# Optimization experiments

Hardware: AMD Instinct MI355X
Metric: run time of the kernel (lower is better)

Reference implementation:

```python
import jax, jax.numpy as jnp
import numpy as np

B, H, OUT, L_LAYERS = 64, 1024, 512, 2
SEQ = 256
SOS_VALUE = -2.0  # predict_binary_output=False


def setup_inputs() -> dict:
    key = jax.random.key(0)
    ks = jax.random.split(key, 16)
    s_ih0 = 1.0 / np.sqrt(OUT)
    s_h = 1.0 / np.sqrt(H)
    return {
        "encoder_output": jax.random.normal(ks[0], (B, SEQ, OUT), jnp.float32),
        "h0": jax.random.normal(ks[1], (L_LAYERS, B, H), jnp.float32),
        "c0": jax.random.normal(ks[2], (L_LAYERS, B, H), jnp.float32),
        "W_ih0": jax.random.normal(ks[3], (4 * H, OUT), jnp.float32) * s_ih0,
        "W_hh0": jax.random.normal(ks[4], (4 * H, H), jnp.float32) * s_h,
        "b_ih0": jax.random.normal(ks[5], (4 * H,), jnp.float32) * s_h,
        "b_hh0": jax.random.normal(ks[6], (4 * H,), jnp.float32) * s_h,
        "W_ih1": jax.random.normal(ks[7], (4 * H, H), jnp.float32) * s_h,
        "W_hh1": jax.random.normal(ks[8], (4 * H, H), jnp.float32) * s_h,
        "b_ih1": jax.random.normal(ks[9], (4 * H,), jnp.float32) * s_h,
        "b_hh1": jax.random.normal(ks[10], (4 * H,), jnp.float32) * s_h,
        "W_fc": jax.random.normal(ks[11], (OUT, H), jnp.float32) * s_h,
        "b_fc": jax.random.normal(ks[12], (OUT,), jnp.float32) * s_h,
        "seq_length": SEQ,
    }


def _lstm_cell(x, h, c, Wih, Whh, bih, bhh):
    # PyTorch gate order: i, f, g, o
    gates = x @ Wih.T + h @ Whh.T + (bih + bhh)
    i, f, g, o = jnp.split(gates, 4, axis=-1)
    i = jax.nn.sigmoid(i)
    f = jax.nn.sigmoid(f)
    g = jnp.tanh(g)
    o = jax.nn.sigmoid(o)
    c_new = f * c + i * g
    h_new = o * jnp.tanh(c_new)
    return h_new, c_new


def reference(encoder_output, h0, c0, W_ih0, W_hh0, b_ih0, b_hh0,
              W_ih1, W_hh1, b_ih1, b_hh1, W_fc, b_fc, seq_length):
    batch = h0.shape[1]
    y_init = jnp.full((batch, OUT), SOS_VALUE, dtype=h0.dtype)  # SOS token
    layers = ((W_ih0, W_hh0, b_ih0, b_hh0), (W_ih1, W_hh1, b_ih1, b_hh1))

    def step(carry, _):
        h, c, y = carry  # h, c: (num_layers, B, H); y: (B, OUT)
        x = y
        hs, cs = [], []
        for l, (Wih, Whh, bih, bhh) in enumerate(layers):
            h_l, c_l = _lstm_cell(x, h[l], c[l], Wih, Whh, bih, bhh)
            hs.append(h_l)
            cs.append(c_l)
            x = h_l
        y_hat = jax.nn.relu(x @ W_fc.T + b_fc)
        return (jnp.stack(hs), jnp.stack(cs), y_hat), y_hat

    (_, _, _), ys = jax.lax.scan(step, (h0, c0, y_init), None, length=seq_length)
    return jnp.transpose(ys, (1, 0, 2))  # (B, seq_length, OUT)
```

## Files before the change

kernel.cpp:

```cpp
#include <hip/hip_runtime.h>
#include <stdint.h>


#define NBLK 256
#define NTHR 256
#define HDIM 1024
#define ODIM 512
#define BDIM 64
#define SEQL 256

typedef _Float16 v8h __attribute__((ext_vector_type(8)));
typedef float    v4f __attribute__((ext_vector_type(4)));

#define WL0_NS 48
#define WL1_NS 64
#define WFC_NS 32
#define WL0_OFF 0
#define WL1_OFF (WL0_NS*1024)
#define WFC_OFF (WL1_OFF + WL1_NS*1024)
#define SMEM_BYTES (WFC_OFF + WFC_NS*1024)

#define YB_SZ  (BDIM*ODIM*2)
#define HB_SZ  (BDIM*HDIM*2)

#define FH0_REL 0
#define FH1_REL (4*256*4)
#define FY_REL  (FH1_REL + 4*256*4)
#define EH0_REL (FY_REL + 4*256*4)
#define EH1_REL (EH0_REL + 4*8*64)
#define EY_REL  (EH1_REL + 4*8*64)
#define FLG_BYTES (EY_REL + 4*8*64)

__device__ __forceinline__ float fsig(float x)   { return 1.0f / (1.0f + __expf(-x)); }
__device__ __forceinline__ float ftanhf(float x) { return 1.0f - 2.0f / (__expf(2.0f*x) + 1.0f); }

__device__ __forceinline__ unsigned long long ald8(const void* p){
  return __hip_atomic_load((const unsigned long long*)p, __ATOMIC_RELAXED, __HIP_MEMORY_SCOPE_AGENT);
}
__device__ __forceinline__ unsigned int ald4(const void* p){
  return __hip_atomic_load((const unsigned int*)p, __ATOMIC_RELAXED, __HIP_MEMORY_SCOPE_AGENT);
}
__device__ __forceinline__ void ast4(void* p, unsigned int v){
  __hip_atomic_store((unsigned int*)p, v, __ATOMIC_RELAXED, __HIP_MEMORY_SCOPE_AGENT);
}

__device__ __forceinline__ void wrap_inv(){
  asm volatile("s_waitcnt vmcnt(0)\n\tbuffer_inv sc1" ::: "memory");
}

__device__ __forceinline__ void wait_word(const unsigned int* w, unsigned int tag){
  while (ald4(w) < tag) __builtin_amdgcn_s_sleep(1);
  asm volatile("" ::: "memory");
}

__device__ __forceinline__ void scan256_pub(const unsigned int* rowf, unsigned int* ew,
                                            unsigned int tag){
  const char* p = (const char*)(rowf + (threadIdx.x & 63)*4);
  while (true){
    unsigned long long a = ald8(p);
    unsigned long long b = ald8(p+8);
    unsigned int m0 = (unsigned int)a, m1 = (unsigned int)(a >> 32);
    unsigned int m2 = (unsigned int)b, m3 = (unsigned int)(b >> 32);
    unsigned int m = min(min(m0, m1), min(m2, m3));
    if (__all(m >= tag)) break;
    __builtin_amdgcn_s_sleep(1);
  }
  if ((threadIdx.x & 63) == 0) ast4(ew, tag);
  asm volatile("" ::: "memory");
}

__device__ __forceinline__ void publish(unsigned int* flag, unsigned int tag){
  asm volatile("s_waitcnt vmcnt(0)" ::: "memory");
  if ((threadIdx.x & 63) == 0) ast4(flag, tag);
}

template<int NC>
__device__ __forceinline__ v4f gemm_phase(const char* const cb[], const char* wl, v4f acc){
  v8h A[4][8];
  constexpr int PF = (NC < 3) ? NC : 3;
  #pragma unroll
  for (int p = 0; p < PF; p++){
    #pragma unroll
    for (int j = 0; j < 8; j++) A[p][j] = *(const v8h*)(cb[p] + (size_t)j*64);
  }
  #pragma unroll
  for (int c = 0; c < NC; c++){
    const int cur = c & 3, nx = (c + 3) & 3;
    if (c + 3 < NC){
      #pragma unroll
      for (int j = 0; j < 8; j++) A[nx][j] = *(const v8h*)(cb[c+3] + (size_t)j*64);
    }
    #pragma unroll
    for (int j = 0; j < 8; j++){
      v8h B = *(const v8h*)(wl + (size_t)(c*8 + j)*1024);
      acc = __builtin_amdgcn_mfma_f32_16x16x32_f16(A[cur][j], B, acc, 0, 0, 0);
    }
  }
  return acc;
}

__device__ __forceinline__ void gemm_dual4(const char* const cb[], const char* wlA,
                                           const char* wlB, v4f& accA, v4f& accB){
  v8h A[4][8];
  #pragma unroll
  for (int p = 0; p < 3; p++){
    #pragma unroll
    for (int j = 0; j < 8; j++) A[p][j] = *(const v8h*)(cb[p] + (size_t)j*64);
  }
  #pragma unroll
  for (int c = 0; c < 4; c++){
    const int cur = c & 3, nx = (c + 3) & 3;
    if (c + 3 < 4){
      #pragma unroll
      for (int j = 0; j < 8; j++) A[nx][j] = *(const v8h*)(cb[c+3] + (size_t)j*64);
    }
    #pragma unroll
    for (int j = 0; j < 8; j++){
      v8h BA = *(const v8h*)(wlA + (size_t)(c*8 + j)*1024);
      accA = __builtin_amdgcn_mfma_f32_16x16x32_f16(A[cur][j], BA, accA, 0, 0, 0);
      v8h BB = *(const v8h*)(wlB + (size_t)(c*8 + j)*1024);
      accB = __builtin_amdgcn_mfma_f32_16x16x32_f16(A[cur][j], BB, accB, 0, 0, 0);
    }
  }
}

__device__ __forceinline__ void lstm_epi_pack(v4f acc, float bias, float* cs,
                                              char* hbase, int l15, int gidx){
  #pragma unroll
  for (int r = 0; r < 4; r++){
    float v  = acc[r] + bias;
    float x1 = __shfl_xor(v, 1);
    float x2 = __shfl_xor(v, 2);
    float x3 = __shfl_xor(v, 3);
    float vi = (gidx==0)?v :(gidx==1)?x1:(gidx==2)?x2:x3;
    float vf = (gidx==1)?v :(gidx==0)?x1:(gidx==3)?x2:x3;
    float vg = (gidx==2)?v :(gidx==3)?x1:(gidx==0)?x2:x3;
    float vo = (gidx==3)?v :(gidx==2)?x1:(gidx==1)?x2:x3;
    float ii = fsig(vi), ff = fsig(vf), gg = ftanhf(vg), oo = fsig(vo);
    float cn = ff*cs[r] + ii*gg;
    cs[r] = cn;
    float hn = oo * ftanhf(cn);
    unsigned int uv = (unsigned int)__builtin_bit_cast(unsigned short, (_Float16)hn);
    unsigned int o4 = (unsigned int)__shfl_xor((int)uv, 4);
    unsigned int pr = uv | (o4 << 16);
    unsigned int o8 = (unsigned int)__shfl_xor((int)pr, 8);
    if (l15 == 0){
      unsigned long long full = (unsigned long long)pr | ((unsigned long long)o8 << 32);
      __hip_atomic_store((unsigned long long*)(hbase + (size_t)r*(HDIM*2)), full,
                         __ATOMIC_RELAXED, __HIP_MEMORY_SCOPE_AGENT);
    }
  }
}

__global__ void init_kernel(const float* __restrict__ h0,
                            _Float16* __restrict__ h0bi, _Float16* __restrict__ h1bi,
                            _Float16* __restrict__ ybi){
  int i = blockIdx.x*256 + threadIdx.x;
  if (i < BDIM*HDIM){
    h0bi[i] = (_Float16)h0[i];
    h1bi[i] = (_Float16)h0[BDIM*HDIM + i];
  }
  if (i < BDIM*ODIM) ybi[i] = (_Float16)(-2.0f);
}

__launch_bounds__(NTHR, 1)
__global__ void decoder_kernel(
    const float* __restrict__ Wih0, const float* __restrict__ Whh0,
    const float* __restrict__ bih0, const float* __restrict__ bhh0,
    const float* __restrict__ Wih1, const float* __restrict__ Whh1,
    const float* __restrict__ bih1, const float* __restrict__ bhh1,
    const float* __restrict__ Wfc,  const float* __restrict__ bfc,
    const float* __restrict__ c0in, float* __restrict__ out,
    char* __restrict__ yB, char* __restrict__ h0B, char* __restrict__ h1B,
    char* __restrict__ flg, int dmask)
{
  extern __shared__ char smem[];
  const int bid = blockIdx.x;
  const int tid = threadIdx.x;
  const int wv  = tid >> 6;
  const int ln  = tid & 63;
  const int l15 = ln & 15;
  const int lq  = ln >> 4;
  const int u0  = bid * 4;
  const int f   = bid & 7;
  const int lead_h0 = (bid < 8);
  const int lead_h1 = (bid >= 8  && bid < 16);
  const int lead_y  = (bid >= 16 && bid < 24);

  unsigned int* fh0r = (unsigned int*)(flg + FH0_REL) + wv*256;
  unsigned int* fh1r = (unsigned int*)(flg + FH1_REL) + wv*256;
  unsigned int* fyr  = (unsigned int*)(flg + FY_REL)  + wv*256;
  unsigned int* eh0  = (unsigned int*)(flg + EH0_REL + (wv*8 + f)*64);
  unsigned int* eh1  = (unsigned int*)(flg + EH1_REL + (wv*8 + f)*64);
  unsigned int* ey   = (unsigned int*)(flg + EY_REL  + (wv*8 + f)*64);

  for (int slot = tid; slot < WL0_NS*64; slot += NTHR){
    int s = slot >> 6, l = slot & 63;
    int r16 = l & 15, q = l >> 4;
    int grow = (r16 & 3)*HDIM + u0 + (r16 >> 2);
    int kb = s*32 + q*8;
    const float* src; int k0;
    if (kb < ODIM){ src = Wih0 + (size_t)grow*ODIM; k0 = kb; }
    else          { src = Whh0 + (size_t)grow*HDIM; k0 = kb - ODIM; }
    v8h hv;
    #pragma unroll
    for (int j = 0; j < 8; j++) hv[j] = (_Float16)src[k0 + j];
    *(v8h*)(smem + WL0_OFF + s*1024 + l*16) = hv;
  }
  for (int slot = tid; slot < WL1_NS*64; slot += NTHR){
    int s = slot >> 6, l = slot & 63;
    int r16 = l & 15, q = l >> 4;
    int grow = (r16 & 3)*HDIM + u0 + (r16 >> 2);
    int kb = s*32 + q*8;
    const float* src; int k0;
    if (kb < HDIM){ src = Wih1 + (size_t)grow*HDIM; k0 = kb; }
    else          { src = Whh1 + (size_t)grow*HDIM; k0 = kb - HDIM; }
    v8h hv;
    #pragma unroll
    for (int j = 0; j < 8; j++) hv[j] = (_Float16)src[k0 + j];
    *(v8h*)(smem + WL1_OFF + s*1024 + l*16) = hv;
  }
  for (int slot = tid; slot < WFC_NS*64; slot += NTHR){
    int s = slot >> 6, l = slot & 63;
    int r16 = l & 15, q = l >> 4;
    int k0 = s*32 + q*8;
    v8h hv;
    if (r16 < 2){
      const float* src = Wfc + (size_t)(bid*2 + r16)*HDIM;
      #pragma unroll
      for (int j = 0; j < 8; j++) hv[j] = (_Float16)src[k0 + j];
    } else {
      #pragma unroll
      for (int j = 0; j < 8; j++) hv[j] = (_Float16)0.0f;
    }
    *(v8h*)(smem + WFC_OFF + s*1024 + l*16) = hv;
  }
  __syncthreads();

  const int gidx = l15 & 3;
  const int unit = u0 + (l15 >> 2);
  const int growL = gidx*HDIM + unit;
  const float bias0 = bih0[growL] + bhh0[growL];
  const float bias1 = bih1[growL] + bhh1[growL];
  const float biasf = (l15 < 2) ? bfc[bid*2 + l15] : 0.f;

  const int rb = wv*16 + lq*4;
  float cs0[4], cs1[4];
  #pragma unroll
  for (int r = 0; r < 4; r++){
    int b = rb + r;
    cs0[r] = c0in[(size_t)(0*BDIM + b)*HDIM + unit];
    cs1[r] = c0in[(size_t)(1*BDIM + b)*HDIM + unit];
  }

  const int row = wv*16 + l15;
  const size_t aoffY = (size_t)row*ODIM*2 + (size_t)lq*16;
  const size_t aoffH = (size_t)row*HDIM*2 + (size_t)lq*16;
  const size_t hwoff = ((size_t)rb*HDIM + u0)*2;
  const char* wl0 = smem + WL0_OFF + ln*16;
  const char* wl1 = smem + WL1_OFF + ln*16;
  const char* wlf = smem + WFC_OFF + ln*16;
  const char* wl0r = wl0 + 16*1024;
  const char* wl1r = wl1 + 32*1024;

  v4f p0 = {0.f,0.f,0.f,0.f};
  {
    const char* hi = h0B + (size_t)dmask*HB_SZ + aoffH;
    const char* cb[4] = { hi, hi+512, hi+1024, hi+1536 };
    p0 = gemm_phase<4>(cb, wl0r, p0);
  }

  for (int t = 0; t < SEQL; t++){
    const int sp = (t - 1) & dmask;
    const int sc = t & dmask;

    if ((t & dmask) == 0) wrap_inv();

    if (t > 0){
      if (lead_y) scan256_pub(fyr, ey, (unsigned)t);
      else        wait_word(ey, (unsigned)t);
    }

    {
      const char* ysrc = yB + (size_t)sp*YB_SZ + aoffY;
      const char* cb[2] = { ysrc, ysrc+512 };
      v4f acc = gemm_phase<2>(cb, wl0, p0);
      lstm_epi_pack(acc, bias0, cs0, h0B + (size_t)sc*HB_SZ + hwoff, l15, gidx);
    }
    publish(&fh0r[bid], (unsigned)(t+1));

    v4f p1 = {0.f,0.f,0.f,0.f};
    {
      const char* hs = h1B + (size_t)sp*HB_SZ + aoffH;
      const char* cb[4] = { hs, hs+512, hs+1024, hs+1536 };
      p1 = gemm_phase<4>(cb, wl1r, p1);
      if (lead_h0) scan256_pub(fh0r, eh0, (unsigned)(t+1));
      else         wait_word(eh0, (unsigned)(t+1));
    }

    {
      const char* hs = h0B + (size_t)sc*HB_SZ + aoffH;
      const char* cb[4] = { hs, hs+512, hs+1024, hs+1536 };
      v4f np0 = {0.f,0.f,0.f,0.f};
      gemm_dual4(cb, wl1, wl0r, p1, np0);
      lstm_epi_pack(p1, bias1, cs1, h1B + (size_t)sc*HB_SZ + hwoff, l15, gidx);
      p0 = np0;
    }
    publish(&fh1r[bid], (unsigned)(t+1));

    if (lead_h1) scan256_pub(fh1r, eh1, (unsigned)(t+1));
    else         wait_word(eh1, (unsigned)(t+1));

    {
      const char* f1 = h1B + (size_t)sc*HB_SZ + aoffH;
      const char* cb[4] = { f1, f1+512, f1+1024, f1+1536 };
      v4f acc = {0.f,0.f,0.f,0.f};
      acc = gemm_phase<4>(cb, wlf, acc);
      char* ydst = yB + (size_t)sc*YB_SZ;
      #pragma unroll
      for (int r = 0; r < 4; r++){
        float v = fmaxf(acc[r] + biasf, 0.f);
        int b = rb + r;
        unsigned int uv = (unsigned int)__builtin_bit_cast(unsigned short, (_Float16)v);
        unsigned int o1 = (unsigned int)__shfl_xor((int)uv, 1);
        if (l15 == 0){
          unsigned int pr = uv | (o1 << 16);
          ast4(ydst + ((size_t)b*ODIM + bid*2)*2, pr);
        }
        if (l15 < 2) out[((size_t)b*SEQL + t)*ODIM + bid*2 + l15] = v;
      }
    }
    publish(&fyr[bid], (unsigned)(t+1));
  }
}

extern "C" void kernel_launch(void* const* d_in, const int* in_sizes, int n_in,
                              void* d_out, int out_size, void* d_ws, size_t ws_size,
                              hipStream_t stream){
  (void)in_sizes; (void)n_in; (void)out_size;

  int D = 16;
  while (D > 2 && (size_t)D*(YB_SZ + 2*HB_SZ) + FLG_BYTES > ws_size) D >>= 1;
  if ((size_t)D*(YB_SZ + 2*HB_SZ) + FLG_BYTES > ws_size) return;

  char* ws  = (char*)d_ws;
  char* yB  = ws;
  char* h0B = yB + (size_t)D*YB_SZ;
  char* h1B = h0B + (size_t)D*HB_SZ;
  char* flg = h1B + (size_t)D*HB_SZ;

  const float* h0   = (const float*)d_in[1];
  const float* c0   = (const float*)d_in[2];
  const float* Wih0 = (const float*)d_in[3];
  const float* Whh0 = (const float*)d_in[4];
  const float* bih0 = (const float*)d_in[5];
  const float* bhh0 = (const float*)d_in[6];
  const float* Wih1 = (const float*)d_in[7];
  const float* Whh1 = (const float*)d_in[8];
  const float* bih1 = (const float*)d_in[9];
  const float* bhh1 = (const float*)d_in[10];
  const float* Wfc  = (const float*)d_in[11];
  const float* bfc  = (const float*)d_in[12];
  float* out = (float*)d_out;

  (void)hipMemsetAsync(flg, 0, FLG_BYTES, stream);
  hipLaunchKernelGGL(init_kernel, dim3(256), dim3(256), 0, stream,
                     h0,
                     (_Float16*)(h0B + (size_t)(D-1)*HB_SZ),
                     (_Float16*)(h1B + (size_t)(D-1)*HB_SZ),
                     (_Float16*)(yB  + (size_t)(D-1)*YB_SZ));

  (void)hipFuncSetAttribute((const void*)decoder_kernel,
                            hipFuncAttributeMaxDynamicSharedMemorySize, SMEM_BYTES);
  hipLaunchKernelGGL(decoder_kernel, dim3(NBLK), dim3(NTHR), SMEM_BYTES, stream,
                     Wih0, Whh0, bih0, bhh0, Wih1, Whh1, bih1, bhh1,
                     Wfc, bfc, c0, out, yB, h0B, h1B, flg, D - 1);
}
```

Measured before the change: 4.919 ms.

## Replicate FC output across 8 block groups to replace global y barrier with local flags

The FC layer is now computed redundantly by 8 replica groups: each block computes 16 output columns instead of 2 and writes them into its own replica of the y buffer. Each layer-0 consumer then waits only on the 32 producers of its replica, not on a two-level scan and broadcast over all 256 blocks. This shortens the per-step synchronisation chain. The cost is 8x FC MFMA work, 8x y buffer memory and more workspace per slot. The fused dual GEMM for layer 1 and the next step's layer-0 recurrent term is also split, so h1 is published before the layer-0 precompute runs.

```diff
diff --git a/kernel.cpp b/kernel.cpp
--- a/kernel.cpp
+++ b/kernel.cpp
@@ -22,14 +22,14 @@
 
 #define YB_SZ  (BDIM*ODIM*2)
 #define HB_SZ  (BDIM*HDIM*2)
+#define SLOTSET (8*YB_SZ + 2*HB_SZ)
 
 #define FH0_REL 0
 #define FH1_REL (4*256*4)
-#define FY_REL  (FH1_REL + 4*256*4)
-#define EH0_REL (FY_REL + 4*256*4)
+#define FYX_REL (FH1_REL + 4*256*4)
+#define EH0_REL (FYX_REL + 8*4*32*4)
 #define EH1_REL (EH0_REL + 4*8*64)
-#define EY_REL  (EH1_REL + 4*8*64)
-#define FLG_BYTES (EY_REL + 4*8*64)
+#define FLG_BYTES (EH1_REL + 4*8*64)
 
 __device__ __forceinline__ float fsig(float x)   { return 1.0f / (1.0f + __expf(-x)); }
 __device__ __forceinline__ float ftanhf(float x) { return 1.0f - 2.0f / (__expf(2.0f*x) + 1.0f); }
@@ -69,6 +69,12 @@
   asm volatile("" ::: "memory");
 }
 
+__device__ __forceinline__ void scan_fyx(const unsigned int* rowf, unsigned int tag){
+  const unsigned int* p = rowf + (threadIdx.x & 31);
+  while (!__all(ald4(p) >= tag)) __builtin_amdgcn_s_sleep(1);
+  asm volatile("" ::: "memory");
+}
+
 __device__ __forceinline__ void publish(unsigned int* flag, unsigned int tag){
   asm volatile("s_waitcnt vmcnt(0)" ::: "memory");
   if ((threadIdx.x & 63) == 0) ast4(flag, tag);
@@ -97,31 +103,6 @@
     }
   }
   return acc;
-}
-
-__device__ __forceinline__ void gemm_dual4(const char* const cb[], const char* wlA,
-                                           const char* wlB, v4f& accA, v4f& accB){
-  v8h A[4][8];
-  #pragma unroll
-  for (int p = 0; p < 3; p++){
-    #pragma unroll
-    for (int j = 0; j < 8; j++) A[p][j] = *(const v8h*)(cb[p] + (size_t)j*64);
-  }
-  #pragma unroll
-  for (int c = 0; c < 4; c++){
-    const int cur = c & 3, nx = (c + 3) & 3;
-    if (c + 3 < 4){
-      #pragma unroll
-      for (int j = 0; j < 8; j++) A[nx][j] = *(const v8h*)(cb[c+3] + (size_t)j*64);
-    }
-    #pragma unroll
-    for (int j = 0; j < 8; j++){
-      v8h BA = *(const v8h*)(wlA + (size_t)(c*8 + j)*1024);
-      accA = __builtin_amdgcn_mfma_f32_16x16x32_f16(A[cur][j], BA, accA, 0, 0, 0);
-      v8h BB = *(const v8h*)(wlB + (size_t)(c*8 + j)*1024);
-      accB = __builtin_amdgcn_mfma_f32_16x16x32_f16(A[cur][j], BB, accB, 0, 0, 0);
-    }
-  }
 }
 
 __device__ __forceinline__ void lstm_epi_pack(v4f acc, float bias, float* cs,
@@ -160,7 +141,10 @@
     h0bi[i] = (_Float16)h0[i];
     h1bi[i] = (_Float16)h0[BDIM*HDIM + i];
   }
-  if (i < BDIM*ODIM) ybi[i] = (_Float16)(-2.0f);
+  if (i < BDIM*ODIM){
+    #pragma unroll
+    for (int x = 0; x < 8; x++) ybi[(size_t)x*(BDIM*ODIM) + i] = (_Float16)(-2.0f);
+  }
 }
 
 __launch_bounds__(NTHR, 1)
@@ -171,7 +155,7 @@
     const float* __restrict__ bih1, const float* __restrict__ bhh1,
     const float* __restrict__ Wfc,  const float* __restrict__ bfc,
     const float* __restrict__ c0in, float* __restrict__ out,
-    char* __restrict__ yB, char* __restrict__ h0B, char* __restrict__ h1B,
+    char* __restrict__ yX, char* __restrict__ h0B, char* __restrict__ h1B,
     char* __restrict__ flg, int dmask)
 {
   extern __shared__ char smem[];
@@ -183,16 +167,17 @@
   const int lq  = ln >> 4;
   const int u0  = bid * 4;
   const int f   = bid & 7;
+  const int j32 = bid >> 3;
+  const int dimb = j32 * 16;
   const int lead_h0 = (bid < 8);
-  const int lead_h1 = (bid >= 8  && bid < 16);
-  const int lead_y  = (bid >= 16 && bid < 24);
+  const int lead_h1 = (bid >= 8 && bid < 16);
+  const int outw = (f == 0);
 
   unsigned int* fh0r = (unsigned int*)(flg + FH0_REL) + wv*256;
   unsigned int* fh1r = (unsigned int*)(flg + FH1_REL) + wv*256;
-  unsigned int* fyr  = (unsigned int*)(flg + FY_REL)  + wv*256;
+  unsigned int* fyxr = (unsigned int*)(flg + FYX_REL) + (f*4 + wv)*32;
   unsigned int* eh0  = (unsigned int*)(flg + EH0_REL + (wv*8 + f)*64);
   unsigned int* eh1  = (unsigned int*)(flg + EH1_REL + (wv*8 + f)*64);
-  unsigned int* ey   = (unsigned int*)(flg + EY_REL  + (wv*8 + f)*64);
 
   for (int slot = tid; slot < WL0_NS*64; slot += NTHR){
     int s = slot >> 6, l = slot & 63;
@@ -223,16 +208,11 @@
   for (int slot = tid; slot < WFC_NS*64; slot += NTHR){
     int s = slot >> 6, l = slot & 63;
     int r16 = l & 15, q = l >> 4;
+    const float* src = Wfc + (size_t)(dimb + r16)*HDIM;
     int k0 = s*32 + q*8;
     v8h hv;
-    if (r16 < 2){
-      const float* src = Wfc + (size_t)(bid*2 + r16)*HDIM;
-      #pragma unroll
-      for (int j = 0; j < 8; j++) hv[j] = (_Float16)src[k0 + j];
-    } else {
-      #pragma unroll
-      for (int j = 0; j < 8; j++) hv[j] = (_Float16)0.0f;
-    }
+    #pragma unroll
+    for (int j = 0; j < 8; j++) hv[j] = (_Float16)src[k0 + j];
     *(v8h*)(smem + WFC_OFF + s*1024 + l*16) = hv;
   }
   __syncthreads();
@@ -242,7 +222,7 @@
   const int growL = gidx*HDIM + unit;
   const float bias0 = bih0[growL] + bhh0[growL];
   const float bias1 = bih1[growL] + bhh1[growL];
-  const float biasf = (l15 < 2) ? bfc[bid*2 + l15] : 0.f;
+  const float biasf = bfc[dimb + l15];
 
   const int rb = wv*16 + lq*4;
   float cs0[4], cs1[4];
@@ -276,13 +256,10 @@
 
     if ((t & dmask) == 0) wrap_inv();
 
-    if (t > 0){
-      if (lead_y) scan256_pub(fyr, ey, (unsigned)t);
-      else        wait_word(ey, (unsigned)t);
-    }
-
-    {
-      const char* ysrc = yB + (size_t)sp*YB_SZ + aoffY;
+    if (t > 0) scan_fyx(fyxr, (unsigned)t);
+
+    {
+      const char* ysrc = yX + ((size_t)sp*8 + f)*YB_SZ + aoffY;
       const char* cb[2] = { ysrc, ysrc+512 };
       v4f acc = gemm_phase<2>(cb, wl0, p0);
       lstm_epi_pack(acc, bias0, cs0, h0B + (size_t)sc*HB_SZ + hwoff, l15, gidx);
@@ -301,36 +278,53 @@
     {
       const char* hs = h0B + (size_t)sc*HB_SZ + aoffH;
       const char* cb[4] = { hs, hs+512, hs+1024, hs+1536 };
+      p1 = gemm_phase<4>(cb, wl1, p1);
+      lstm_epi_pack(p1, bias1, cs1, h1B + (size_t)sc*HB_SZ + hwoff, l15, gidx);
+    }
+    publish(&fh1r[bid], (unsigned)(t+1));
+
+    {
+      const char* hs = h0B + (size_t)sc*HB_SZ + aoffH;
+      const char* cb[4] = { hs, hs+512, hs+1024, hs+1536 };
       v4f np0 = {0.f,0.f,0.f,0.f};
-      gemm_dual4(cb, wl1, wl0r, p1, np0);
-      lstm_epi_pack(p1, bias1, cs1, h1B + (size_t)sc*HB_SZ + hwoff, l15, gidx);
+      np0 = gemm_phase<4>(cb, wl0r, np0);
       p0 = np0;
     }
-    publish(&fh1r[bid], (unsigned)(t+1));
-
     if (lead_h1) scan256_pub(fh1r, eh1, (unsigned)(t+1));
     else         wait_word(eh1, (unsigned)(t+1));
 
+    float yv[4];
     {
       const char* f1 = h1B + (size_t)sc*HB_SZ + aoffH;
       const char* cb[4] = { f1, f1+512, f1+1024, f1+1536 };
       v4f acc = {0.f,0.f,0.f,0.f};
       acc = gemm_phase<4>(cb, wlf, acc);
-      char* ydst = yB + (size_t)sc*YB_SZ;
+      char* ydst = yX + ((size_t)sc*8 + f)*YB_SZ;
       #pragma unroll
       for (int r = 0; r < 4; r++){
         float v = fmaxf(acc[r] + biasf, 0.f);
+        yv[r] = v;
         int b = rb + r;
         unsigned int uv = (unsigned int)__builtin_bit_cast(unsigned short, (_Float16)v);
         unsigned int o1 = (unsigned int)__shfl_xor((int)uv, 1);
-        if (l15 == 0){
-          unsigned int pr = uv | (o1 << 16);
-          ast4(ydst + ((size_t)b*ODIM + bid*2)*2, pr);
+        unsigned int pr = uv | (o1 << 16);
+        unsigned int o2 = (unsigned int)__shfl_xor((int)pr, 2);
+        if ((l15 & 3) == 0){
+          unsigned long long full = (unsigned long long)pr | ((unsigned long long)o2 << 32);
+          __hip_atomic_store((unsigned long long*)(ydst + ((size_t)b*ODIM + dimb + l15)*2),
+                             full, __ATOMIC_RELAXED, __HIP_MEMORY_SCOPE_AGENT);
         }
-        if (l15 < 2) out[((size_t)b*SEQL + t)*ODIM + bid*2 + l15] = v;
       }
     }
-    publish(&fyr[bid], (unsigned)(t+1));
+    publish(&fyxr[j32], (unsigned)(t+1));
+
+    if (outw){
+      #pragma unroll
+      for (int r = 0; r < 4; r++){
+        int b = rb + r;
+        out[((size_t)b*SEQL + t)*ODIM + dimb + l15] = yv[r];
+      }
+    }
   }
 }
 
@@ -340,12 +334,12 @@
   (void)in_sizes; (void)n_in; (void)out_size;
 
   int D = 16;
-  while (D > 2 && (size_t)D*(YB_SZ + 2*HB_SZ) + FLG_BYTES > ws_size) D >>= 1;
-  if ((size_t)D*(YB_SZ + 2*HB_SZ) + FLG_BYTES > ws_size) return;
+  while (D > 2 && (size_t)D*SLOTSET + FLG_BYTES > ws_size) D >>= 1;
+  if ((size_t)D*SLOTSET + FLG_BYTES > ws_size) return;
 
   char* ws  = (char*)d_ws;
-  char* yB  = ws;
-  char* h0B = yB + (size_t)D*YB_SZ;
+  char* yX  = ws;
+  char* h0B = yX + (size_t)D*8*YB_SZ;
   char* h1B = h0B + (size_t)D*HB_SZ;
   char* flg = h1B + (size_t)D*HB_SZ;
 
@@ -368,11 +362,11 @@
                      h0,
                      (_Float16*)(h0B + (size_t)(D-1)*HB_SZ),
                      (_Float16*)(h1B + (size_t)(D-1)*HB_SZ),
-                     (_Float16*)(yB  + (size_t)(D-1)*YB_SZ));
+                     (_Float16*)(yX  + (size_t)(D-1)*8*YB_SZ));
 
   (void)hipFuncSetAttribute((const void*)decoder_kernel,
                             hipFuncAttributeMaxDynamicSharedMemorySize, SMEM_BYTES);
   hipLaunchKernelGGL(decoder_kernel, dim3(NBLK), dim3(NTHR), SMEM_BYTES, stream,
                      Wih0, Whh0, bih0, bhh0, Wih1, Whh1, bih1, bhh1,
-                     Wfc, bfc, c0, out, yB, h0B, h1B, flg, D - 1);
-}
+                     Wfc, bfc, c0, out, yX, h0B, h1B, flg, D - 1);
+}
```

Result: slower. 6.950 ms (+41.3%).

## Publish layer-1 h before next-step layer-0 GEMM and defer output stores

Applied to the files above, without the earlier changes.

The fused dual GEMM that computed layer-1 gates and the next step's layer-0 recurrent partial together is split into two passes. Layer-1 h is now computed and published first, and the layer-0 partial GEMM runs while the barrier scan/wait on h1 is in flight. The global output store is moved after the y-flag publish, so other blocks are released sooner. The cost is reading the h0 A-operands twice instead of sharing them across both GEMMs.

```diff
diff --git a/kernel.cpp b/kernel.cpp
--- a/kernel.cpp
+++ b/kernel.cpp
@@ -97,31 +97,6 @@
     }
   }
   return acc;
-}
-
-__device__ __forceinline__ void gemm_dual4(const char* const cb[], const char* wlA,
-                                           const char* wlB, v4f& accA, v4f& accB){
-  v8h A[4][8];
-  #pragma unroll
-  for (int p = 0; p < 3; p++){
-    #pragma unroll
-    for (int j = 0; j < 8; j++) A[p][j] = *(const v8h*)(cb[p] + (size_t)j*64);
-  }
-  #pragma unroll
-  for (int c = 0; c < 4; c++){
-    const int cur = c & 3, nx = (c + 3) & 3;
-    if (c + 3 < 4){
-      #pragma unroll
-      for (int j = 0; j < 8; j++) A[nx][j] = *(const v8h*)(cb[c+3] + (size_t)j*64);
-    }
-    #pragma unroll
-    for (int j = 0; j < 8; j++){
-      v8h BA = *(const v8h*)(wlA + (size_t)(c*8 + j)*1024);
-      accA = __builtin_amdgcn_mfma_f32_16x16x32_f16(A[cur][j], BA, accA, 0, 0, 0);
-      v8h BB = *(const v8h*)(wlB + (size_t)(c*8 + j)*1024);
-      accB = __builtin_amdgcn_mfma_f32_16x16x32_f16(A[cur][j], BB, accB, 0, 0, 0);
-    }
-  }
 }
 
 __device__ __forceinline__ void lstm_epi_pack(v4f acc, float bias, float* cs,
@@ -301,16 +276,26 @@
     {
       const char* hs = h0B + (size_t)sc*HB_SZ + aoffH;
       const char* cb[4] = { hs, hs+512, hs+1024, hs+1536 };
+      p1 = gemm_phase<4>(cb, wl1, p1);
+      lstm_epi_pack(p1, bias1, cs1, h1B + (size_t)sc*HB_SZ + hwoff, l15, gidx);
+    }
+    publish(&fh1r[bid], (unsigned)(t+1));
+
+    {
+      const char* hs = h0B + (size_t)sc*HB_SZ + aoffH;
+      const char* cb[4] = { hs, hs+512, hs+1024, hs+1536 };
       v4f np0 = {0.f,0.f,0.f,0.f};
-      gemm_dual4(cb, wl1, wl0r, p1, np0);
-      lstm_epi_pack(p1, bias1, cs1, h1B + (size_t)sc*HB_SZ + hwoff, l15, gidx);
+      if (lead_h1){
+        scan256_pub(fh1r, eh1, (unsigned)(t+1));
+        np0 = gemm_phase<4>(cb, wl0r, np0);
+      } else {
+        np0 = gemm_phase<4>(cb, wl0r, np0);
+        wait_word(eh1, (unsigned)(t+1));
+      }
       p0 = np0;
     }
-    publish(&fh1r[bid], (unsigned)(t+1));
-
-    if (lead_h1) scan256_pub(fh1r, eh1, (unsigned)(t+1));
-    else         wait_word(eh1, (unsigned)(t+1));
-
+
+    float yv[4];
     {
       const char* f1 = h1B + (size_t)sc*HB_SZ + aoffH;
       const char* cb[4] = { f1, f1+512, f1+1024, f1+1536 };
@@ -320,6 +305,7 @@
       #pragma unroll
       for (int r = 0; r < 4; r++){
         float v = fmaxf(acc[r] + biasf, 0.f);
+        yv[r] = v;
         int b = rb + r;
         unsigned int uv = (unsigned int)__builtin_bit_cast(unsigned short, (_Float16)v);
         unsigned int o1 = (unsigned int)__shfl_xor((int)uv, 1);
@@ -327,10 +313,15 @@
           unsigned int pr = uv | (o1 << 16);
           ast4(ydst + ((size_t)b*ODIM + bid*2)*2, pr);
         }
-        if (l15 < 2) out[((size_t)b*SEQL + t)*ODIM + bid*2 + l15] = v;
       }
     }
     publish(&fyr[bid], (unsigned)(t+1));
+
+    #pragma unroll
+    for (int r = 0; r < 4; r++){
+      int b = rb + r;
+      if (l15 < 2) out[((size_t)b*SEQL + t)*ODIM + bid*2 + l15] = yv[r];
+    }
   }
 }
 
```

Result: slower. 5.830 ms (+18.5%).
